# Optimization experiments

Measured on AMD Instinct MI355X. Metric: run time of the kernel, lower is better.

The kernel has to match this reference:

```python
import jax, jax.numpy as jnp
import numpy as np


def _conv(x, w, stride=1, pad=0):
    return jax.lax.conv_general_dilated(
        x, w, window_strides=(stride, stride),
        padding=[(pad, pad), (pad, pad)],
        dimension_numbers=('NCHW', 'OIHW', 'NCHW'))


def _frozen_bn(x, gamma, beta, mean, var):
    # FrozenBatchNorm2d: scale = gamma * rsqrt(var); bias = beta - mean*scale
    scale = gamma * jax.lax.rsqrt(var)
    bias = beta - mean * scale
    return x * scale[None, :, None, None] + bias[None, :, None, None]


def setup_inputs() -> dict:
    key = jax.random.key(0)
    ks = jax.random.split(key, 16)
    N, Cin, H, W = 32, 1024, 28, 28
    Cb, Cout = 256, 1024
    x = jax.random.normal(ks[0], (N, Cin, H, W), dtype=jnp.float32)
    # conv weights, kaiming-uniform-ish scale
    w1 = jax.random.uniform(ks[1], (Cb, Cin, 1, 1), minval=-1, maxval=1) * (1.0 / np.sqrt(Cin))
    w2 = jax.random.uniform(ks[2], (Cb, Cb, 3, 3), minval=-1, maxval=1) * (1.0 / np.sqrt(Cb * 9))
    w3 = jax.random.uniform(ks[3], (Cout, Cb, 1, 1), minval=-1, maxval=1) * (1.0 / np.sqrt(Cb))
    def bn_params(k, n):
        k1, k2, k3, k4 = jax.random.split(k, 4)
        gamma = jax.random.uniform(k1, (n,), minval=0.5, maxval=1.5)
        beta = jax.random.normal(k2, (n,)) * 0.1
        mean = jax.random.normal(k3, (n,)) * 0.1
        var = jax.random.uniform(k4, (n,), minval=0.5, maxval=1.5)
        return gamma, beta, mean, var
    g1, b1, m1, v1 = bn_params(ks[4], Cb)
    g2, b2, m2, v2 = bn_params(ks[5], Cb)
    g3, b3, m3, v3 = bn_params(ks[6], Cout)
    return dict(x=x, w1=w1, w2=w2, w3=w3,
                g1=g1, b1=b1, m1=m1, v1=v1,
                g2=g2, b2=b2, m2=m2, v2=v2,
                g3=g3, b3=b3, m3=m3, v3=v3)


def reference(x, w1, w2, w3, g1, b1, m1, v1, g2, b2, m2, v2, g3, b3, m3, v3):
    identity = x
    out = _conv(x, w1, stride=1, pad=0)          # 1x1: Cin -> Cb
    out = jax.nn.relu(_frozen_bn(out, g1, b1, m1, v1))
    out = _conv(out, w2, stride=1, pad=1)        # 3x3: Cb -> Cb
    out = jax.nn.relu(_frozen_bn(out, g2, b2, m2, v2))
    out = _conv(out, w3, stride=1, pad=0)        # 1x1: Cb -> Cout
    out = _frozen_bn(out, g3, b3, m3, v3)
    # stride==1 and in_channels==out_channels -> downsample is None
    out = jax.nn.relu(out + identity)
    return out
```

## Files before the change

### kernel.cpp

```cpp
#include <hip/hip_runtime.h>
#include <hip/hip_bf16.h>


#define BK 64
#define WAITVM(N) asm volatile("s_waitcnt vmcnt(" #N ")" ::: "memory")

typedef __attribute__((ext_vector_type(8))) short short8;
typedef __attribute__((ext_vector_type(4))) float f32x4;

__device__ inline unsigned short f2bf(float f) {
    unsigned int u = __float_as_uint(f);
    u += 0x7fff + ((u >> 16) & 1);
    return (unsigned short)(u >> 16);
}

__device__ inline unsigned cvt_pk_bf16(float a, float b) {
    __hip_bfloat162 h = __float22bfloat162_rn(make_float2(a, b));
    return *reinterpret_cast<unsigned*>(&h);
}

__device__ inline void gload16(const unsigned short* g, unsigned short* l) {
    __builtin_amdgcn_global_load_lds(
        (const __attribute__((address_space(1))) unsigned int*)g,
        (__attribute__((address_space(3))) unsigned int*)l, 16, 0, 0);
}

__global__ __launch_bounds__(256) void prep_w(
    const float* __restrict__ w1, const float* __restrict__ w2, const float* __restrict__ w3,
    const float* g1, const float* b1, const float* m1, const float* v1,
    const float* g2, const float* b2, const float* m2, const float* v2,
    const float* g3, const float* b3, const float* m3, const float* v3,
    unsigned short* __restrict__ Wb1, unsigned short* __restrict__ Wt2,
    unsigned short* __restrict__ Wb3,
    float* __restrict__ bn1, float* __restrict__ bn2, float* __restrict__ bn3,
    uint4* __restrict__ y1p) {
    int i = blockIdx.x * 256 + threadIdx.x;
    if (i < 262144) Wb1[i] = f2bf(w1[i]);
    if (i < 589824) {
        int kw = i % 3, t1 = i / 3;
        int kh = t1 % 3, t2 = t1 / 3;
        int ci = t2 & 255, co = t2 >> 8;
        Wt2[(size_t)((kh * 3 + kw) * 256 + co) * 256 + ci] = f2bf(w2[i]);
    }
    if (i < 262144) Wb3[i] = f2bf(w3[i]);
    if (i < 256) { float s = g1[i] * rsqrtf(v1[i]); bn1[i] = s; bn1[256 + i] = b1[i] - m1[i] * s; }
    if (i < 256) { float s = g2[i] * rsqrtf(v2[i]); bn2[i] = s; bn2[256 + i] = b2[i] - m2[i] * s; }
    if (i < 1024) { float s = g3[i] * rsqrtf(v3[i]); bn3[i] = s; bn3[1024 + i] = b3[i] - m3[i] * s; }
    if (i < 118784) {
        int ch8 = i & 31;
        int t = i >> 5;
        int cell = t % 116;
        int n = t / 116;
        int h, w;
        if (cell < 30)      { h = 0;          w = cell; }
        else if (cell < 60) { h = 29;         w = cell - 30; }
        else if (cell < 88) { h = cell - 59;  w = 0; }
        else                { h = cell - 87;  w = 29; }
        y1p[((size_t)n * 900 + h * 30 + w) * 32 + ch8] = make_uint4(0u, 0u, 0u, 0u);
    }
}

template <int CX, int NTAPS, int LAYER, int NT, int BMT>
__device__ __forceinline__ void conv_body(
    const float* __restrict__ Xf,
    const unsigned short* __restrict__ Xg, const unsigned short* __restrict__ Wg,
    const float* __restrict__ bn, int nco,
    const float* __restrict__ residual,
    unsigned short* __restrict__ obf, float* __restrict__ ofp) {
    constexpr int KSTEPS = CX / BK;
    constexpr int NSTEP = NTAPS * KSTEPS;
    constexpr int XB = BMT * BK * 2;
    constexpr int WB = NT * BK * 2;
    constexpr int STAGEB = 2 * (XB + WB);
    constexpr int EPIB = (LAYER == 3) ? 64 * 132 * 4 : 64 * (NT + 8) * 2;
    constexpr int SMEMB = STAGEB > EPIB ? STAGEB : EPIB;
    constexpr int NWJ = BMT / 32;
    constexpr int WR = NT / 32;
    constexpr int XR = BMT / 32;

    __shared__ __align__(16) char smem[SMEMB];
    unsigned short* const Xs0 = (unsigned short*)smem;
    unsigned short* const Xs1 = (unsigned short*)(smem + XB);
    unsigned short* const Ws0 = (unsigned short*)(smem + 2 * XB);
    unsigned short* const Ws1 = (unsigned short*)(smem + 2 * XB + WB);

    const int tid = threadIdx.x;
    const int wave = tid >> 6, lane = tid & 63;
    const int quad = lane >> 4, l15 = lane & 15;
    const int Pb = blockIdx.x * BMT;
    const int cb = blockIdx.y * NT;
    const int wco = (wave & 1) * 64;
    const int wpx = (wave >> 1) * (BMT / 2);

    size_t wro[WR];
    #pragma unroll
    for (int t = 0; t < WR; ++t) {
        int slot = t * 256 + tid;
        int row = slot >> 3;
        int c = slot & 7;
        wro[t] = (size_t)(cb + row) * CX + ((c ^ (row & 7)) * 8);
    }

    int cso[4];
    size_t xrow[4];
    if (LAYER != 1) {
        #pragma unroll
        for (int t = 0; t < XR; ++t) {
            int slot = t * 256 + tid;
            int row = slot >> 3;
            int c = slot & 7;
            cso[t] = ((c ^ (row & 7)) * 8);
            if (LAYER == 2) {
                int P = Pb + row;
                int n = P / 784, rem = P - n * 784;
                int h = rem / 28, w = rem - h * 28;
                xrow[t] = (size_t)n * 900 + h * 30 + w;
            } else {
                xrow[t] = (size_t)(Pb + row);
            }
        }
    }

    const int cpl = (lane >> 2) + (wave & 1) * 16;
    size_t xbase[2];
    int plr[2];
    if (LAYER == 1) {
        #pragma unroll
        for (int r = 0; r < 2; ++r) {
            int quarter = (wave >> 1) + 2 * r;
            int pl = quarter * 16 + (lane & 3) * 4;
            int P = Pb + pl;
            int n = P / 784, p = P - n * 784;
            plr[r] = pl;
            xbase[r] = ((size_t)n * 1024 + 2 * cpl) * 784 + p;
        }
    }

    auto stageW = [&](int s, unsigned short* wsb) {
        int tap = (NTAPS == 1) ? 0 : (s / KSTEPS);
        int k0 = (s - tap * KSTEPS) * BK;
        const unsigned short* Wtap = Wg + (size_t)tap * 256 * CX;
        #pragma unroll
        for (int t = 0; t < WR; ++t)
            gload16(Wtap + wro[t] + k0, wsb + (t * 256 + wave * 64) * 8);
    };
    auto stageX = [&](int s, unsigned short* xsb) {
        int tap = (NTAPS == 1) ? 0 : (s / KSTEPS);
        int k0 = (s - tap * KSTEPS) * BK;
        int tapofs = (NTAPS == 9) ? ((tap / 3) * 30 + (tap % 3)) : 0;
        #pragma unroll
        for (int t = 0; t < XR; ++t)
            gload16(Xg + (xrow[t] + tapofs) * (size_t)CX + k0 + cso[t],
                    xsb + (t * 256 + wave * 64) * 8);
    };
    float4 xa[2], xb[2];
    auto loadX1 = [&](int s) {
        size_t k0 = (size_t)s * BK;
        #pragma unroll
        for (int r = 0; r < 2; ++r) {
            const float* src = Xf + xbase[r] + k0 * 784;
            xa[r] = *(const float4*)src;
            xb[r] = *(const float4*)(src + 784);
        }
    };
    auto convW1 = [&](unsigned short* xsb) {
        #pragma unroll
        for (int r = 0; r < 2; ++r) {
            float av[4] = {xa[r].x, xa[r].y, xa[r].z, xa[r].w};
            float bv[4] = {xb[r].x, xb[r].y, xb[r].z, xb[r].w};
            #pragma unroll
            for (int j = 0; j < 4; ++j) {
                unsigned u = cvt_pk_bf16(av[j], bv[j]);
                int row = plr[r] + j;
                int dw = row * 32 + (((cpl >> 2) ^ (row & 7)) << 2) + (cpl & 3);
                ((unsigned*)xsb)[dw] = u;
            }
        }
    };

    f32x4 acc[4][NWJ];
    #pragma unroll
    for (int i = 0; i < 4; ++i)
        #pragma unroll
        for (int j = 0; j < NWJ; ++j)
            acc[i][j] = (f32x4){0.f, 0.f, 0.f, 0.f};

    auto compute = [&](const unsigned short* xsb, const unsigned short* wsb) {
        #pragma unroll
        for (int kk = 0; kk < BK; kk += 32) {
            short8 af[4], bf[NWJ];
            const int cbase = kk >> 3;
            #pragma unroll
            for (int wi = 0; wi < 4; ++wi) {
                int row = wco + wi * 16 + l15;
                int ch = (cbase + quad) ^ (row & 7);
                af[wi] = *(const short8*)(wsb + (row * 8 + ch) * 8);
            }
            #pragma unroll
            for (int wj = 0; wj < NWJ; ++wj) {
                int row = wpx + wj * 16 + l15;
                int ch = (cbase + quad) ^ (row & 7);
                bf[wj] = *(const short8*)(xsb + (row * 8 + ch) * 8);
            }
            #pragma unroll
            for (int wi = 0; wi < 4; ++wi)
                #pragma unroll
                for (int wj = 0; wj < NWJ; ++wj)
                    acc[wi][wj] = __builtin_amdgcn_mfma_f32_16x16x32_bf16(
                        af[wi], bf[wj], acc[wi][wj], 0, 0, 0);
        }
    };

    if (LAYER == 1) loadX1(0);
    stageW(0, Ws0);
    if (LAYER == 1) convW1(Xs0);
    else            stageX(0, Xs0);

    int cur = 0;
    #pragma unroll 1
    for (int s = 0; s < NSTEP; ++s) {
        unsigned short* xc = cur ? Xs1 : Xs0;
        unsigned short* wc = cur ? Ws1 : Ws0;
        unsigned short* xn = cur ? Xs0 : Xs1;
        unsigned short* wn = cur ? Ws0 : Ws1;
        const bool pre = (s + 1 < NSTEP);
        if (pre) {
            if (LAYER == 1) loadX1(s + 1);
            stageW(s + 1, wn);
            if (LAYER != 1) stageX(s + 1, xn);
        }
        if (pre) WAITVM(8);
        else     WAITVM(0);
        __builtin_amdgcn_sched_barrier(0);
        __builtin_amdgcn_s_barrier();
        compute(xc, wc);
        if (LAYER == 1 && pre) convW1(xn);
        if (LAYER == 1) asm volatile("s_waitcnt lgkmcnt(0)" ::: "memory");
        __builtin_amdgcn_s_barrier();
        __builtin_amdgcn_sched_barrier(0);
        cur ^= 1;
    }

    __syncthreads();

    if (LAYER == 3) {
        float* ep = (float*)smem;
        #pragma unroll
        for (int pass = 0; pass < 2; ++pass) {
            if ((wave & 1) == pass) {
                #pragma unroll
                for (int wi = 0; wi < 4; ++wi) {
                    int co0 = cb + wco + wi * 16 + quad * 4;
                    f32x4 sc = *(const f32x4*)(bn + co0);
                    f32x4 bi = *(const f32x4*)(bn + nco + co0);
                    int cr0 = wi * 16 + quad * 4;
                    #pragma unroll
                    for (int wj = 0; wj < 4; ++wj) {
                        int px = wpx + wj * 16 + l15;
                        #pragma unroll
                        for (int r = 0; r < 4; ++r)
                            ep[(cr0 + r) * 132 + px] = fmaf(acc[wi][wj][r], sc[r], bi[r]);
                    }
                }
            }
            __syncthreads();
            {
                int cr = tid >> 2;
                int cg = tid & 3;
                int co = cb + pass * 64 + cr;
                #pragma unroll
                for (int k = 0; k < 8; ++k) {
                    int px4 = (cg + 4 * k) * 4;
                    f32x4 v = *(const f32x4*)(ep + cr * 132 + px4);
                    int P = Pb + px4;
                    int n = P / 784, p = P - n * 784;
                    size_t off = ((size_t)n * 1024 + co) * 784 + p;
                    float4 rs = *(const float4*)(residual + off);
                    float4 o;
                    o.x = v[0] + rs.x; o.x = o.x > 0.f ? o.x : 0.f;
                    o.y = v[1] + rs.y; o.y = o.y > 0.f ? o.y : 0.f;
                    o.z = v[2] + rs.z; o.z = o.z > 0.f ? o.z : 0.f;
                    o.w = v[3] + rs.w; o.w = o.w > 0.f ? o.w : 0.f;
                    *(float4*)(ofp + off) = o;
                }
            }
            __syncthreads();
        }
    } else {
        constexpr int NPASS = BMT / 64;
        constexpr int EPW = NT + 8;
        unsigned short* ep = (unsigned short*)smem;
        #pragma unroll
        for (int pass = 0; pass < NPASS; ++pass) {
            if (NPASS == 1 || (wave >> 1) == pass) {
                #pragma unroll
                for (int wi = 0; wi < 4; ++wi) {
                    int co0 = cb + wco + wi * 16 + quad * 4;
                    f32x4 sc = *(const f32x4*)(bn + co0);
                    f32x4 bi = *(const f32x4*)(bn + nco + co0);
                    int col = wco + wi * 16 + quad * 4;
                    #pragma unroll
                    for (int wj = 0; wj < NWJ; ++wj) {
                        int pxl = (wpx & 63) + wj * 16 + l15;
                        float v0 = fmaf(acc[wi][wj][0], sc[0], bi[0]); v0 = v0 > 0.f ? v0 : 0.f;
                        float v1 = fmaf(acc[wi][wj][1], sc[1], bi[1]); v1 = v1 > 0.f ? v1 : 0.f;
                        float v2 = fmaf(acc[wi][wj][2], sc[2], bi[2]); v2 = v2 > 0.f ? v2 : 0.f;
                        float v3 = fmaf(acc[wi][wj][3], sc[3], bi[3]); v3 = v3 > 0.f ? v3 : 0.f;
                        uint2 pk;
                        pk.x = cvt_pk_bf16(v0, v1);
                        pk.y = cvt_pk_bf16(v2, v3);
                        *(uint2*)(ep + pxl * EPW + col) = pk;
                    }
                }
            }
            __syncthreads();
            {
                int pxl = tid >> 2;
                int cg = tid & 3;
                int P = Pb + pass * 64 + pxl;
                size_t orow;
                if (LAYER == 1) {
                    int n = P / 784, rem = P - n * 784;
                    int h = rem / 28, w = rem - h * 28;
                    orow = (size_t)n * 900 + (h + 1) * 30 + (w + 1);
                } else {
                    orow = (size_t)P;
                }
                #pragma unroll
                for (int k = 0; k < NT / 32; ++k) {
                    int cc = (cg + 4 * k) * 8;
                    uint4 v = *(const uint4*)(ep + pxl * EPW + cc);
                    *(uint4*)(obf + orow * 256 + cb + cc) = v;
                }
            }
            if (pass + 1 < NPASS) __syncthreads();
        }
    }
}

__global__ __launch_bounds__(256) void conv1_mfma(
    const float* __restrict__ Xf, const unsigned short* __restrict__ Wg,
    const float* __restrict__ bn, unsigned short* __restrict__ obf) {
    conv_body<1024, 1, 1, 128, 64>(Xf, nullptr, Wg, bn, 256, nullptr, obf, nullptr);
}
__global__ __launch_bounds__(256) void conv2_mfma(
    const unsigned short* __restrict__ Xg, const unsigned short* __restrict__ Wg,
    const float* __restrict__ bn, unsigned short* __restrict__ obf) {
    conv_body<256, 9, 2, 128, 128>(nullptr, Xg, Wg, bn, 256, nullptr, obf, nullptr);
}
__global__ __launch_bounds__(256) void conv3_mfma(
    const unsigned short* __restrict__ Xg, const unsigned short* __restrict__ Wg,
    const float* __restrict__ bn, const float* __restrict__ residual,
    float* __restrict__ ofp) {
    conv_body<256, 1, 3, 128, 128>(nullptr, Xg, Wg, bn, 1024, residual, nullptr, ofp);
}

extern "C" void kernel_launch(void* const* d_in, const int* in_sizes, int n_in,
                              void* d_out, int out_size, void* d_ws, size_t ws_size,
                              hipStream_t stream) {
    const float* x  = (const float*)d_in[0];
    const float* w1 = (const float*)d_in[1];
    const float* w2 = (const float*)d_in[2];
    const float* w3 = (const float*)d_in[3];
    const float* g1 = (const float*)d_in[4];  const float* b1 = (const float*)d_in[5];
    const float* m1 = (const float*)d_in[6];  const float* v1 = (const float*)d_in[7];
    const float* g2 = (const float*)d_in[8];  const float* b2 = (const float*)d_in[9];
    const float* m2 = (const float*)d_in[10]; const float* v2 = (const float*)d_in[11];
    const float* g3 = (const float*)d_in[12]; const float* b3 = (const float*)d_in[13];
    const float* m3 = (const float*)d_in[14]; const float* v3 = (const float*)d_in[15];
    float* out = (float*)d_out;

    char* ws = (char*)d_ws;
    unsigned short* y1p = (unsigned short*)(ws);
    unsigned short* y2  = (unsigned short*)(ws + 14745600);
    unsigned short* Wb1 = (unsigned short*)(ws + 27590656);
    unsigned short* Wt2 = (unsigned short*)(ws + 28114944);
    unsigned short* Wb3 = (unsigned short*)(ws + 29294592);
    float* bn1 = (float*)(ws + 29818880);
    float* bn2 = (float*)(ws + 29820928);
    float* bn3 = (float*)(ws + 29822976);

    prep_w<<<2304, 256, 0, stream>>>(w1, w2, w3,
                                     g1, b1, m1, v1, g2, b2, m2, v2, g3, b3, m3, v3,
                                     Wb1, Wt2, Wb3, bn1, bn2, bn3, (uint4*)y1p);

    conv1_mfma<<<dim3(392, 2), 256, 0, stream>>>(x, Wb1, bn1, y1p);
    conv2_mfma<<<dim3(196, 2), 256, 0, stream>>>(y1p, Wt2, bn2, y2);
    conv3_mfma<<<dim3(196, 8), 256, 0, stream>>>(y2, Wb3, bn3, x, out);
}
```

Before: 303.4 us.

## Prefetch layer-1 fp32 activations two steps ahead with ping-pong registers

In layer 1, the fp32 activation loads are now issued two K-steps ahead into alternating register sets, and the loop is manually unrolled by two. The intent is to hide global-load latency before the bf16 conversion into LDS, which previously waited on loads issued only one step earlier. The wait counts are adjusted to match. This costs extra registers, which may reduce occupancy, and relies on NSTEP being even, or on the predicate handling, to stay correct.

Result: no change. 303.5 us (+0.0%).

```diff
diff --git a/kernel.cpp b/kernel.cpp
--- a/kernel.cpp
+++ b/kernel.cpp
@@ -153,8 +153,8 @@
             gload16(Xg + (xrow[t] + tapofs) * (size_t)CX + k0 + cso[t],
                     xsb + (t * 256 + wave * 64) * 8);
     };
-    float4 xa[2], xb[2];
-    auto loadX1 = [&](int s) {
+    float4 xaE[2], xbE[2], xaO[2], xbO[2];
+    auto loadX1_to = [&](int s, float4 (&xa)[2], float4 (&xb)[2]) {
         size_t k0 = (size_t)s * BK;
         #pragma unroll
         for (int r = 0; r < 2; ++r) {
@@ -163,7 +163,8 @@
             xb[r] = *(const float4*)(src + 784);
         }
     };
-    auto convW1 = [&](unsigned short* xsb) {
+    auto convW1_from = [&](const float4 (&xa)[2], const float4 (&xb)[2],
+                           unsigned short* xsb) {
         #pragma unroll
         for (int r = 0; r < 2; ++r) {
             float av[4] = {xa[r].x, xa[r].y, xa[r].z, xa[r].w};
@@ -211,34 +212,86 @@
         }
     };
 
-    if (LAYER == 1) loadX1(0);
-    stageW(0, Ws0);
-    if (LAYER == 1) convW1(Xs0);
-    else            stageX(0, Xs0);
-
-    int cur = 0;
-    #pragma unroll 1
-    for (int s = 0; s < NSTEP; ++s) {
-        unsigned short* xc = cur ? Xs1 : Xs0;
-        unsigned short* wc = cur ? Ws1 : Ws0;
-        unsigned short* xn = cur ? Xs0 : Xs1;
-        unsigned short* wn = cur ? Ws0 : Ws1;
-        const bool pre = (s + 1 < NSTEP);
-        if (pre) {
-            if (LAYER == 1) loadX1(s + 1);
-            stageW(s + 1, wn);
-            if (LAYER != 1) stageX(s + 1, xn);
-        }
-        if (pre) WAITVM(8);
-        else     WAITVM(0);
-        __builtin_amdgcn_sched_barrier(0);
-        __builtin_amdgcn_s_barrier();
-        compute(xc, wc);
-        if (LAYER == 1 && pre) convW1(xn);
-        if (LAYER == 1) asm volatile("s_waitcnt lgkmcnt(0)" ::: "memory");
-        __builtin_amdgcn_s_barrier();
-        __builtin_amdgcn_sched_barrier(0);
-        cur ^= 1;
+    if constexpr (LAYER == 1) {
+        loadX1_to(0, xaE, xbE);
+        loadX1_to(1, xaO, xbO);
+        stageW(0, Ws0);
+        convW1_from(xaE, xbE, Xs0);
+        int cur = 0;
+        #pragma unroll 1
+        for (int s = 0; s < NSTEP; s += 2) {
+            {
+                unsigned short* xc = cur ? Xs1 : Xs0;
+                unsigned short* wc = cur ? Ws1 : Ws0;
+                unsigned short* xn = cur ? Xs0 : Xs1;
+                unsigned short* wn = cur ? Ws0 : Ws1;
+                const bool pre = (s + 1 < NSTEP);
+                const bool pre2 = (s + 2 < NSTEP);
+                if (pre2) loadX1_to(s + 2, xaE, xbE);
+                if (pre) stageW(s + 1, wn);
+                if (pre2) WAITVM(8);
+                else if (pre) WAITVM(4);
+                else WAITVM(0);
+                __builtin_amdgcn_sched_barrier(0);
+                __builtin_amdgcn_s_barrier();
+                compute(xc, wc);
+                if (pre) {
+                    convW1_from(xaO, xbO, xn);
+                    asm volatile("s_waitcnt lgkmcnt(0)" ::: "memory");
+                }
+                __builtin_amdgcn_s_barrier();
+                __builtin_amdgcn_sched_barrier(0);
+                cur ^= 1;
+            }
+            {
+                const int t = s + 1;
+                unsigned short* xc = cur ? Xs1 : Xs0;
+                unsigned short* wc = cur ? Ws1 : Ws0;
+                unsigned short* xn = cur ? Xs0 : Xs1;
+                unsigned short* wn = cur ? Ws0 : Ws1;
+                const bool pre = (t + 1 < NSTEP);
+                const bool pre2 = (t + 2 < NSTEP);
+                if (pre2) loadX1_to(t + 2, xaO, xbO);
+                if (pre) stageW(t + 1, wn);
+                if (pre2) WAITVM(8);
+                else if (pre) WAITVM(4);
+                else WAITVM(0);
+                __builtin_amdgcn_sched_barrier(0);
+                __builtin_amdgcn_s_barrier();
+                compute(xc, wc);
+                if (pre) {
+                    convW1_from(xaE, xbE, xn);
+                    asm volatile("s_waitcnt lgkmcnt(0)" ::: "memory");
+                }
+                __builtin_amdgcn_s_barrier();
+                __builtin_amdgcn_sched_barrier(0);
+                cur ^= 1;
+            }
+        }
+    } else {
+        stageW(0, Ws0);
+        stageX(0, Xs0);
+        int cur = 0;
+        #pragma unroll 1
+        for (int s = 0; s < NSTEP; ++s) {
+            unsigned short* xc = cur ? Xs1 : Xs0;
+            unsigned short* wc = cur ? Ws1 : Ws0;
+            unsigned short* xn = cur ? Xs0 : Xs1;
+            unsigned short* wn = cur ? Ws0 : Ws1;
+            const bool pre = (s + 1 < NSTEP);
+            if (pre) {
+                stageW(s + 1, wn);
+                stageX(s + 1, xn);
+            }
+            if (pre) WAITVM(8);
+            else     WAITVM(0);
+            __builtin_amdgcn_sched_barrier(0);
+            __builtin_amdgcn_s_barrier();
+            compute(xc, wc);
+            __builtin_amdgcn_s_barrier();
+            __builtin_amdgcn_sched_barrier(0);
+            cur ^= 1;
+        }
     }
 
     __syncthreads();
```
